# Performance work log

Measured on AMD Instinct MI355X. Metric: run time of the kernel, lower is better.

The kernel has to match this reference:

```python
import jax, jax.numpy as jnp
import numpy as np

VOCAB = 50000
EMB = 128
HID = 128
BEAM = 4
MAXLEN = 24
B = 16
TENC = 64
START_IDX = 2


def setup_inputs() -> dict:
    key = jax.random.key(0)
    ks = jax.random.split(key, 9)
    s = 0.05
    return {
        "encoder_output": jax.random.normal(ks[0], (B, TENC, 2 * HID), jnp.float32),
        "initial_hidden": jax.random.normal(ks[1], (2, B, HID), jnp.float32),
        "embedding": jax.random.normal(ks[2], (VOCAB, EMB), jnp.float32) * s,
        "W_ih": jax.random.normal(ks[3], (3 * HID, EMB), jnp.float32) * s,
        "W_hh": jax.random.normal(ks[4], (3 * HID, HID), jnp.float32) * s,
        "b_ih": jnp.zeros((3 * HID,), jnp.float32),
        "b_hh": jnp.zeros((3 * HID,), jnp.float32),
        "W_logit": jax.random.normal(ks[5], (VOCAB, 2 * HID), jnp.float32) * s,
        "b_logit": jnp.zeros((VOCAB,), jnp.float32),
    }


def _gru_cell(x, h, W_ih, W_hh, b_ih, b_hh):
    # x: [k,B,E], h: [k,B,H]; torch gate order: r, z, n
    gi = x @ W_ih.T + b_ih
    gh = h @ W_hh.T + b_hh
    ir, iz, inn = jnp.split(gi, 3, axis=-1)
    hr, hz, hn = jnp.split(gh, 3, axis=-1)
    r = jax.nn.sigmoid(ir + hr)
    z = jax.nn.sigmoid(iz + hz)
    n = jnp.tanh(inn + r * hn)
    return (1.0 - z) * n + z * h


def _decode(encoder_output, initial_hidden, embedding, W_ih, W_hh, b_ih, b_hh, W_logit, b_logit):
    # take forward-direction encoder states: view(B,T,2,H)[:,:,0,:]
    enc_fwd = encoder_output.reshape(B, TENC, 2, HID)[:, :, 0, :]  # [B,T,H]
    # initial_hidden.view(num_layers=1, 2, B, H)[:,0] -> single-layer fwd hidden
    h0 = initial_hidden.reshape(1, 2, B, HID)[0, 0]  # [B,H]
    k_h0 = jnp.broadcast_to(h0, (BEAM, B, HID))
    k_pred0 = jnp.full((BEAM, B), START_IDX, dtype=jnp.int32)
    k_lps0 = jnp.zeros((BEAM, B), jnp.float32)

    def step(carry, _):
        last_pred, h, lps = carry
        emb = embedding[last_pred]                      # [k,B,E]
        h_new = _gru_cell(emb, h, W_ih, W_hh, b_ih, b_hh)  # [k,B,H]
        out = h_new
        # inline dot attention over forward encoder states
        scores = jnp.einsum('bth,kbh->kbt', enc_fwd, out)      # [k,B,T]
        probs = jax.nn.softmax(scores, axis=-1)
        attn = jnp.einsum('kbt,bth->kbh', probs, enc_fwd)      # [k,B,H]
        feat = jnp.concatenate([attn, out], axis=-1)           # [k,B,2H]
        logits = feat @ W_logit.T + b_logit                    # [k,B,V]
        lsm = jax.nn.log_softmax(logits, axis=-1)
        lps_full = lsm + lps[:, :, None]                       # [k,B,V]
        flat = lps_full.transpose(1, 0, 2).reshape(B, BEAM * VOCAB)
        vals, idx = jax.lax.top_k(flat, BEAM)                  # [B,k]
        beam_idx = idx // VOCAB                                # [B,k]
        tok = (idx % VOCAB).astype(jnp.int32)                  # [B,k]
        # re-sort beam-major tensors by chosen parent beam
        h_b = jnp.take_along_axis(h_new.transpose(1, 0, 2), beam_idx[:, :, None], axis=1).transpose(1, 0, 2)
        lsm_b = jnp.take_along_axis(lsm.transpose(1, 0, 2), beam_idx[:, :, None], axis=1).transpose(1, 0, 2)
        new_carry = (tok.T, h_b, vals.T)
        return new_carry, (lsm_b, tok.T, beam_idx)

    _, (lsm_all, preds_all, parents_all) = jax.lax.scan(
        step, (k_pred0, k_h0, k_lps0), None, length=MAXLEN)
    # lsm_all: [T,k,B,V], preds_all: [T,k,B], parents_all: [T,B,k]

    bidx = jnp.arange(B)

    def back(parent, xs):
        lsm_t, preds_t, parents_t = xs
        out = lsm_t[parent, bidx]          # [B,V]
        pr = preds_t[parent, bidx]         # [B]
        new_parent = parents_t[bidx, parent]
        return new_parent, (out, pr)

    _, (outs, prs) = jax.lax.scan(back, jnp.zeros((B,), jnp.int32),
                                  (lsm_all, preds_all, parents_all), reverse=True)
    return outs, prs  # [T,B,V] log-softmax, [T,B] token ids


def reference(encoder_output, initial_hidden, embedding, W_ih, W_hh, b_ih, b_hh, W_logit, b_logit):
    return _decode(encoder_output, initial_hidden, embedding, W_ih, W_hh, b_ih, b_hh, W_logit, b_logit)
```

## Files before the change

### kernel.cpp

```cpp
#include <hip/hip_runtime.h>
#include <math.h>
#include <float.h>

#define VOCABSZ 50000
#define EMBSZ 128
#define HIDSZ 128
#define BSZ 16
#define TENCSZ 64
#define STEPSN 24
#define STARTTOK 2
#define RPB 64
#define NBLK 782

#define FEAT_OFF 0
#define HBUF_OFF (STEPSN*BSZ*256)
#define CBUF_OFF (HBUF_OFF + BSZ*HIDSZ)
#define PMAX_OFF (CBUF_OFF + STEPSN*BSZ)
#define PSUM_OFF (PMAX_OFF + NBLK*BSZ)
#define WS_FLOATS (PSUM_OFF + NBLK*BSZ)

__global__ __launch_bounds__(256) void step_kernel(
    const float* __restrict__ Wl, const float* __restrict__ bl,
    const float* __restrict__ ws_f_c, float* __restrict__ ws_f,
    int* __restrict__ ws_i, float* __restrict__ out, int t)
{
  const int tid = threadIdx.x;
  const int lane = tid & 63;
  const int waveu = __builtin_amdgcn_readfirstlane(tid >> 6);
  const int r0 = waveu * 4;
  const int v = blockIdx.x * RPB + lane;
  const bool valid = v < VOCABSZ;

  const float* feat_t = ws_f_c + FEAT_OFF + (size_t)t * BSZ * 256;
  const float4* __restrict__ fb = (const float4*)(feat_t + r0 * 256);
  const float4* __restrict__ wrow = (const float4*)(Wl + (size_t)(valid ? v : 0) * 256);

  float a0 = 0.f, a1 = 0.f, a2 = 0.f, a3 = 0.f;
#pragma unroll 4
  for (int k = 0; k < 64; ++k) {
    float4 w = wrow[k];
    float4 f0 = fb[k];
    float4 f1 = fb[64 + k];
    float4 f2 = fb[128 + k];
    float4 f3 = fb[192 + k];
    a0 += f0.x * w.x + f0.y * w.y + f0.z * w.z + f0.w * w.w;
    a1 += f1.x * w.x + f1.y * w.y + f1.z * w.z + f1.w * w.w;
    a2 += f2.x * w.x + f2.y * w.y + f2.z * w.z + f2.w * w.w;
    a3 += f3.x * w.x + f3.y * w.y + f3.z * w.z + f3.w * w.w;
  }
  const float lb = valid ? bl[v] : 0.f;
  float lg[4] = {a0 + lb, a1 + lb, a2 + lb, a3 + lb};

  if (valid) {
#pragma unroll
    for (int j = 0; j < 4; ++j)
      out[((size_t)t * BSZ + (r0 + j)) * VOCABSZ + v] = lg[j];
    if (t > 0) {
      const float* cb = ws_f_c + CBUF_OFF + (t - 1) * BSZ;
#pragma unroll
      for (int j = 0; j < 4; ++j) {
        size_t idx = ((size_t)(t - 1) * BSZ + (r0 + j)) * VOCABSZ + v;
        out[idx] = out[idx] - cb[r0 + j];
      }
    }
  }

  float* pmax = ws_f + PMAX_OFF;
  float* psum = ws_f + PSUM_OFF;
  int* pidx = ws_i;
#pragma unroll
  for (int j = 0; j < 4; ++j) {
    float m = valid ? lg[j] : -FLT_MAX;
    int mi = valid ? v : 0x7fffffff;
#pragma unroll
    for (int off = 32; off; off >>= 1) {
      float om = __shfl_xor(m, off);
      int oi = __shfl_xor(mi, off);
      if (om > m || (om == m && oi < mi)) { m = om; mi = oi; }
    }
    float s = valid ? expf(lg[j] - m) : 0.f;
#pragma unroll
    for (int off = 32; off; off >>= 1) s += __shfl_xor(s, off);
    if (lane == 0) {
      pmax[(r0 + j) * NBLK + blockIdx.x] = m;
      psum[(r0 + j) * NBLK + blockIdx.x] = s;
      pidx[(r0 + j) * NBLK + blockIdx.x] = mi;
    }
  }
}

__global__ __launch_bounds__(256) void rg_kernel(
    const float* __restrict__ enc, const float* __restrict__ inith,
    const float* __restrict__ embed,
    const float* __restrict__ W_ih, const float* __restrict__ W_hh,
    const float* __restrict__ b_ih, const float* __restrict__ b_hh,
    float* __restrict__ ws_f, int* __restrict__ ws_i,
    float* __restrict__ out, int rstep, int gstep)
{
  const int b = blockIdx.x, tid = threadIdx.x;
  float* feat = ws_f + FEAT_OFF;
  float* hbuf = ws_f + HBUF_OFF;
  float* cbuf = ws_f + CBUF_OFF;
  float* pmax = ws_f + PMAX_OFF;
  float* psum = ws_f + PSUM_OFF;
  int* pidx = ws_i;

  __shared__ float s_wm[4]; __shared__ int s_wi[4];
  __shared__ float s_ws[4];
  __shared__ int s_tok;
  __shared__ float s_emb[EMBSZ];
  __shared__ float s_h[HIDSZ];
  __shared__ float s_hnew[HIDSZ];
  __shared__ float s_gh[3 * HIDSZ];
  __shared__ float s_probs[TENCSZ];

  const int lane = tid & 63, wave = tid >> 6;

  if (rstep >= 0) {
    float m = -FLT_MAX; int mi = 0x7fffffff;
    for (int i = tid; i < NBLK; i += 256) {
      float mm = pmax[b * NBLK + i]; int ii = pidx[b * NBLK + i];
      if (mm > m || (mm == m && ii < mi)) { m = mm; mi = ii; }
    }
#pragma unroll
    for (int off = 32; off; off >>= 1) {
      float om = __shfl_xor(m, off); int oi = __shfl_xor(mi, off);
      if (om > m || (om == m && oi < mi)) { m = om; mi = oi; }
    }
    if (lane == 0) { s_wm[wave] = m; s_wi[wave] = mi; }
    __syncthreads();
    float gm = s_wm[0]; int gi_ = s_wi[0];
#pragma unroll
    for (int w = 1; w < 4; ++w) {
      if (s_wm[w] > gm || (s_wm[w] == gm && s_wi[w] < gi_)) { gm = s_wm[w]; gi_ = s_wi[w]; }
    }
    float e = 0.f;
    for (int i = tid; i < NBLK; i += 256)
      e += psum[b * NBLK + i] * expf(pmax[b * NBLK + i] - gm);
#pragma unroll
    for (int off = 32; off; off >>= 1) e += __shfl_xor(e, off);
    if (lane == 0) s_ws[wave] = e;
    __syncthreads();
    if (tid == 0) {
      float tot = s_ws[0] + s_ws[1] + s_ws[2] + s_ws[3];
      cbuf[rstep * BSZ + b] = gm + logf(tot);
      out[(size_t)STEPSN * BSZ * VOCABSZ + rstep * BSZ + b] = (float)gi_;
      s_tok = gi_;
    }
    __syncthreads();
  }

  if (gstep >= 0) {
    const int tok = (gstep == 0) ? STARTTOK : s_tok;
    if (tid < 128) {
      s_emb[tid] = embed[(size_t)tok * EMBSZ + tid];
      s_h[tid] = (gstep == 0) ? inith[b * HIDSZ + tid] : hbuf[b * HIDSZ + tid];
    }
    __syncthreads();
    float gr = 0.f, gz = 0.f, gn = 0.f;
    if (tid < 128) {
      gr = b_ih[tid]; gz = b_ih[tid + 128]; gn = b_ih[tid + 256];
      const float* wr = W_ih + (size_t)tid * EMBSZ;
      const float* wz = W_ih + (size_t)(tid + 128) * EMBSZ;
      const float* wn = W_ih + (size_t)(tid + 256) * EMBSZ;
      for (int k = 0; k < EMBSZ; ++k) {
        float e = s_emb[k];
        gr += wr[k] * e; gz += wz[k] * e; gn += wn[k] * e;
      }
    } else {
      int j = tid - 128;
      float hr = b_hh[j], hz = b_hh[j + 128], hn = b_hh[j + 256];
      const float* wr = W_hh + (size_t)j * HIDSZ;
      const float* wz = W_hh + (size_t)(j + 128) * HIDSZ;
      const float* wn = W_hh + (size_t)(j + 256) * HIDSZ;
      for (int k = 0; k < HIDSZ; ++k) {
        float h = s_h[k];
        hr += wr[k] * h; hz += wz[k] * h; hn += wn[k] * h;
      }
      s_gh[j] = hr; s_gh[128 + j] = hz; s_gh[256 + j] = hn;
    }
    __syncthreads();
    if (tid < 128) {
      float r = 1.f / (1.f + expf(-(gr + s_gh[tid])));
      float z = 1.f / (1.f + expf(-(gz + s_gh[128 + tid])));
      float n = tanhf(gn + r * s_gh[256 + tid]);
      s_hnew[tid] = (1.f - z) * n + z * s_h[tid];
    }
    __syncthreads();
    if (tid < 64) {
      const float* ep = enc + ((size_t)b * TENCSZ + tid) * 256;
      float sc = 0.f;
      for (int k = 0; k < HIDSZ; ++k) sc += ep[k] * s_hnew[k];
      float mx = sc;
#pragma unroll
      for (int off = 32; off; off >>= 1) mx = fmaxf(mx, __shfl_xor(mx, off));
      float p = expf(sc - mx);
      float su = p;
#pragma unroll
      for (int off = 32; off; off >>= 1) su += __shfl_xor(su, off);
      s_probs[tid] = p / su;
    }
    __syncthreads();
    if (tid < 128) {
      float a = 0.f;
      for (int tt = 0; tt < TENCSZ; ++tt)
        a += s_probs[tt] * enc[((size_t)b * TENCSZ + tt) * 256 + tid];
      float* fptr = feat + ((size_t)gstep * BSZ + b) * 256;
      fptr[tid] = a;
      fptr[128 + tid] = s_hnew[tid];
      hbuf[b * HIDSZ + tid] = s_hnew[tid];
    }
  }
}

__global__ __launch_bounds__(256) void sub_last_kernel(
    const float* __restrict__ cbuf, float* __restrict__ out)
{
  size_t i = ((size_t)blockIdx.x * 256 + threadIdx.x) * 8;
  if (i >= (size_t)BSZ * VOCABSZ) return;
  int b = (int)(i / VOCABSZ);
  float c = cbuf[(STEPSN - 1) * BSZ + b];
  float4* p = (float4*)(out + (size_t)(STEPSN - 1) * BSZ * VOCABSZ + i);
  float4 x0 = p[0], x1 = p[1];
  x0.x -= c; x0.y -= c; x0.z -= c; x0.w -= c;
  x1.x -= c; x1.y -= c; x1.z -= c; x1.w -= c;
  p[0] = x0; p[1] = x1;
}

extern "C" void kernel_launch(void* const* d_in, const int* in_sizes, int n_in,
                              void* d_out, int out_size, void* d_ws, size_t ws_size,
                              hipStream_t stream)
{
  const float* enc   = (const float*)d_in[0];
  const float* inith = (const float*)d_in[1];
  const float* embed = (const float*)d_in[2];
  const float* W_ih  = (const float*)d_in[3];
  const float* W_hh  = (const float*)d_in[4];
  const float* b_ih  = (const float*)d_in[5];
  const float* b_hh  = (const float*)d_in[6];
  const float* Wl    = (const float*)d_in[7];
  const float* bl    = (const float*)d_in[8];
  float* out = (float*)d_out;

  float* ws_f = (float*)d_ws;
  int* ws_i = (int*)(ws_f + WS_FLOATS);

  rg_kernel<<<BSZ, 256, 0, stream>>>(enc, inith, embed, W_ih, W_hh, b_ih, b_hh,
                                     ws_f, ws_i, out, -1, 0);
  for (int t = 0; t < STEPSN; ++t) {
    step_kernel<<<NBLK, 256, 0, stream>>>(Wl, bl, ws_f, ws_f, ws_i, out, t);
    rg_kernel<<<BSZ, 256, 0, stream>>>(enc, inith, embed, W_ih, W_hh, b_ih, b_hh,
                                       ws_f, ws_i, out, t, (t < STEPSN - 1) ? (t + 1) : -1);
  }
  const int nsub = (BSZ * VOCABSZ / 8 + 255) / 256;
  sub_last_kernel<<<nsub, 256, 0, stream>>>(ws_f + CBUF_OFF, out);
}
```

Baseline: 1.355 ms.

## Tile logit GEMV through shared memory and stage encoder states in LDS

The vocab logit kernel now gives each block 128 vocab rows. It stages W_logit tiles in double-buffered shared memory with coalesced float4 loads, and each wave computes 8 batch rows instead of 4. This cuts the uncoalesced per-thread row reads of the weight matrix, halves the block count, and doubles the partial softmax slots per block. The recurrent kernel also copies the forward encoder states into LDS once and runs the attention dot products from there with vector reads. The cost is more shared memory per block, which can lower occupancy, plus an extra sync per K tile.

```diff
diff --git a/kernel.cpp b/kernel.cpp
--- a/kernel.cpp
+++ b/kernel.cpp
@@ -9,58 +9,101 @@
 #define TENCSZ 64
 #define STEPSN 24
 #define STARTTOK 2
-#define RPB 64
-#define NBLK 782
+
+#define RPBK 128
+#define NBLK2 391
+#define NSLOT 782
+#define KT 32
+#define PITCH 36
 
 #define FEAT_OFF 0
 #define HBUF_OFF (STEPSN*BSZ*256)
 #define CBUF_OFF (HBUF_OFF + BSZ*HIDSZ)
 #define PMAX_OFF (CBUF_OFF + STEPSN*BSZ)
-#define PSUM_OFF (PMAX_OFF + NBLK*BSZ)
-#define WS_FLOATS (PSUM_OFF + NBLK*BSZ)
+#define PSUM_OFF (PMAX_OFF + NSLOT*BSZ)
+#define WS_FLOATS (PSUM_OFF + NSLOT*BSZ)
 
 __global__ __launch_bounds__(256) void step_kernel(
     const float* __restrict__ Wl, const float* __restrict__ bl,
-    const float* __restrict__ ws_f_c, float* __restrict__ ws_f,
+    const float* __restrict__ ws_c, float* __restrict__ ws_f,
     int* __restrict__ ws_i, float* __restrict__ out, int t)
 {
+  __shared__ float sW[2][RPBK * PITCH];
   const int tid = threadIdx.x;
   const int lane = tid & 63;
-  const int waveu = __builtin_amdgcn_readfirstlane(tid >> 6);
-  const int r0 = waveu * 4;
-  const int v = blockIdx.x * RPB + lane;
+  const int wv = tid >> 6;
+  const int rowhalf = wv & 1;
+  const int bh0 = __builtin_amdgcn_readfirstlane((wv >> 1) * 8);
+  const int v0 = blockIdx.x * RPBK;
+  const int r = rowhalf * 64 + lane;
+  const int v = v0 + r;
   const bool valid = v < VOCABSZ;
 
-  const float* feat_t = ws_f_c + FEAT_OFF + (size_t)t * BSZ * 256;
-  const float4* __restrict__ fb = (const float4*)(feat_t + r0 * 256);
-  const float4* __restrict__ wrow = (const float4*)(Wl + (size_t)(valid ? v : 0) * 256);
-
-  float a0 = 0.f, a1 = 0.f, a2 = 0.f, a3 = 0.f;
-#pragma unroll 4
-  for (int k = 0; k < 64; ++k) {
-    float4 w = wrow[k];
-    float4 f0 = fb[k];
-    float4 f1 = fb[64 + k];
-    float4 f2 = fb[128 + k];
-    float4 f3 = fb[192 + k];
-    a0 += f0.x * w.x + f0.y * w.y + f0.z * w.z + f0.w * w.w;
-    a1 += f1.x * w.x + f1.y * w.y + f1.z * w.z + f1.w * w.w;
-    a2 += f2.x * w.x + f2.y * w.y + f2.z * w.z + f2.w * w.w;
-    a3 += f3.x * w.x + f3.y * w.y + f3.z * w.z + f3.w * w.w;
-  }
+  const float* feat_t = ws_c + FEAT_OFF + (size_t)t * (BSZ * 256) + bh0 * 256;
+  const float4* __restrict__ Wl4 = (const float4*)Wl;
+
+  int srow[4], sc4[4], gbase[4];
+#pragma unroll
+  for (int i = 0; i < 4; ++i) {
+    int f4lin = i * 256 + tid;
+    srow[i] = f4lin >> 3;
+    sc4[i] = f4lin & 7;
+    int vrow = v0 + srow[i];
+    if (vrow >= VOCABSZ) vrow = VOCABSZ - 1;
+    gbase[i] = vrow * 64 + sc4[i];
+  }
+
+  float acc[8];
+#pragma unroll
+  for (int b = 0; b < 8; ++b) acc[b] = 0.f;
+
+  float4 stg[4];
+#pragma unroll
+  for (int i = 0; i < 4; ++i) stg[i] = Wl4[gbase[i]];
+#pragma unroll
+  for (int i = 0; i < 4; ++i)
+    *(float4*)&sW[0][srow[i] * PITCH + sc4[i] * 4] = stg[i];
+  __syncthreads();
+
+  for (int kt = 0; kt < 8; ++kt) {
+    if (kt < 7) {
+#pragma unroll
+      for (int i = 0; i < 4; ++i) stg[i] = Wl4[gbase[i] + (kt + 1) * 8];
+    }
+    const float* wrow = &sW[kt & 1][r * PITCH];
+    const float* fp = feat_t + kt * KT;
+#pragma unroll
+    for (int k4 = 0; k4 < 8; ++k4) {
+      float4 wvv = *(const float4*)&wrow[k4 * 4];
+#pragma unroll
+      for (int b = 0; b < 8; ++b) {
+        float4 f = *(const float4*)(fp + b * 256 + k4 * 4);
+        acc[b] += f.x * wvv.x + f.y * wvv.y + f.z * wvv.z + f.w * wvv.w;
+      }
+    }
+    if (kt < 7) {
+#pragma unroll
+      for (int i = 0; i < 4; ++i)
+        *(float4*)&sW[(kt + 1) & 1][srow[i] * PITCH + sc4[i] * 4] = stg[i];
+      __syncthreads();
+    }
+  }
+
   const float lb = valid ? bl[v] : 0.f;
-  float lg[4] = {a0 + lb, a1 + lb, a2 + lb, a3 + lb};
+  float lg[8];
+#pragma unroll
+  for (int b = 0; b < 8; ++b) lg[b] = acc[b] + lb;
 
   if (valid) {
 #pragma unroll
-    for (int j = 0; j < 4; ++j)
-      out[((size_t)t * BSZ + (r0 + j)) * VOCABSZ + v] = lg[j];
+    for (int b = 0; b < 8; ++b)
+      out[((size_t)t * BSZ + bh0 + b) * VOCABSZ + v] = lg[b];
     if (t > 0) {
-      const float* cb = ws_f_c + CBUF_OFF + (t - 1) * BSZ;
-#pragma unroll
-      for (int j = 0; j < 4; ++j) {
-        size_t idx = ((size_t)(t - 1) * BSZ + (r0 + j)) * VOCABSZ + v;
-        out[idx] = out[idx] - cb[r0 + j];
+      const float* cb = ws_c + CBUF_OFF + (t - 1) * BSZ + bh0;
+#pragma unroll
+      for (int b = 0; b < 8; ++b) {
+        size_t idx = ((size_t)(t - 1) * BSZ + bh0 + b) * VOCABSZ + v;
+        out[idx] = out[idx] - cb[b];
       }
     }
   }
@@ -68,9 +111,10 @@
   float* pmax = ws_f + PMAX_OFF;
   float* psum = ws_f + PSUM_OFF;
   int* pidx = ws_i;
-#pragma unroll
-  for (int j = 0; j < 4; ++j) {
-    float m = valid ? lg[j] : -FLT_MAX;
+  const int slot = blockIdx.x * 2 + rowhalf;
+#pragma unroll
+  for (int b = 0; b < 8; ++b) {
+    float m = valid ? lg[b] : -FLT_MAX;
     int mi = valid ? v : 0x7fffffff;
 #pragma unroll
     for (int off = 32; off; off >>= 1) {
@@ -78,13 +122,13 @@
       int oi = __shfl_xor(mi, off);
       if (om > m || (om == m && oi < mi)) { m = om; mi = oi; }
     }
-    float s = valid ? expf(lg[j] - m) : 0.f;
+    float s = valid ? expf(lg[b] - m) : 0.f;
 #pragma unroll
     for (int off = 32; off; off >>= 1) s += __shfl_xor(s, off);
     if (lane == 0) {
-      pmax[(r0 + j) * NBLK + blockIdx.x] = m;
-      psum[(r0 + j) * NBLK + blockIdx.x] = s;
-      pidx[(r0 + j) * NBLK + blockIdx.x] = mi;
+      pmax[(bh0 + b) * NSLOT + slot] = m;
+      psum[(bh0 + b) * NSLOT + slot] = s;
+      pidx[(bh0 + b) * NSLOT + slot] = mi;
     }
   }
 }
@@ -105,6 +149,7 @@
   float* psum = ws_f + PSUM_OFF;
   int* pidx = ws_i;
 
+  __shared__ float s_enc[64 * 132];
   __shared__ float s_wm[4]; __shared__ int s_wi[4];
   __shared__ float s_ws[4];
   __shared__ int s_tok;
@@ -116,10 +161,20 @@
 
   const int lane = tid & 63, wave = tid >> 6;
 
+  if (gstep >= 0) {
+#pragma unroll
+    for (int i = 0; i < 8; ++i) {
+      int f4lin = i * 256 + tid;
+      int row = f4lin >> 5, c = f4lin & 31;
+      float4 e = ((const float4*)(enc + ((size_t)b * TENCSZ + row) * 256))[c];
+      *(float4*)&s_enc[row * 132 + c * 4] = e;
+    }
+  }
+
   if (rstep >= 0) {
     float m = -FLT_MAX; int mi = 0x7fffffff;
-    for (int i = tid; i < NBLK; i += 256) {
-      float mm = pmax[b * NBLK + i]; int ii = pidx[b * NBLK + i];
+    for (int i = tid; i < NSLOT; i += 256) {
+      float mm = pmax[b * NSLOT + i]; int ii = pidx[b * NSLOT + i];
       if (mm > m || (mm == m && ii < mi)) { m = mm; mi = ii; }
     }
 #pragma unroll
@@ -135,8 +190,8 @@
       if (s_wm[w] > gm || (s_wm[w] == gm && s_wi[w] < gi_)) { gm = s_wm[w]; gi_ = s_wi[w]; }
     }
     float e = 0.f;
-    for (int i = tid; i < NBLK; i += 256)
-      e += psum[b * NBLK + i] * expf(pmax[b * NBLK + i] - gm);
+    for (int i = tid; i < NSLOT; i += 256)
+      e += psum[b * NSLOT + i] * expf(pmax[b * NSLOT + i] - gm);
 #pragma unroll
     for (int off = 32; off; off >>= 1) e += __shfl_xor(e, off);
     if (lane == 0) s_ws[wave] = e;
@@ -188,9 +243,14 @@
     }
     __syncthreads();
     if (tid < 64) {
-      const float* ep = enc + ((size_t)b * TENCSZ + tid) * 256;
+      const float4* ep = (const float4*)&s_enc[tid * 132];
+      const float4* h4 = (const float4*)s_hnew;
       float sc = 0.f;
-      for (int k = 0; k < HIDSZ; ++k) sc += ep[k] * s_hnew[k];
+#pragma unroll
+      for (int k = 0; k < 32; ++k) {
+        float4 e = ep[k], h = h4[k];
+        sc += e.x * h.x + e.y * h.y + e.z * h.z + e.w * h.w;
+      }
       float mx = sc;
 #pragma unroll
       for (int off = 32; off; off >>= 1) mx = fmaxf(mx, __shfl_xor(mx, off));
@@ -203,8 +263,9 @@
     __syncthreads();
     if (tid < 128) {
       float a = 0.f;
+#pragma unroll 8
       for (int tt = 0; tt < TENCSZ; ++tt)
-        a += s_probs[tt] * enc[((size_t)b * TENCSZ + tt) * 256 + tid];
+        a += s_probs[tt] * s_enc[tt * 132 + tid];
       float* fptr = feat + ((size_t)gstep * BSZ + b) * 256;
       fptr[tid] = a;
       fptr[128 + tid] = s_hnew[tid];
@@ -248,7 +309,7 @@
   rg_kernel<<<BSZ, 256, 0, stream>>>(enc, inith, embed, W_ih, W_hh, b_ih, b_hh,
                                      ws_f, ws_i, out, -1, 0);
   for (int t = 0; t < STEPSN; ++t) {
-    step_kernel<<<NBLK, 256, 0, stream>>>(Wl, bl, ws_f, ws_f, ws_i, out, t);
+    step_kernel<<<NBLK2, 256, 0, stream>>>(Wl, bl, ws_f, ws_f, ws_i, out, t);
     rg_kernel<<<BSZ, 256, 0, stream>>>(enc, inith, embed, W_ih, W_hh, b_ih, b_hh,
                                        ws_f, ws_i, out, t, (t < STEPSN - 1) ? (t + 1) : -1);
   }
```

Result: slower. 1.701 ms (+25.5%).

## Fuse per-step reduction and GRU into logit kernel via last-block atomic ticket

Applied to the files above, without the earlier changes.

Merges the separate reduce/GRU kernel into the logit step kernel: each block takes an atomic ticket, and the last 16 blocks spin until all blocks finish, then each performs the argmax/logsumexp reduction and next-step GRU+attention for one batch row. The logit GEMV is restructured so each wave computes 16 vocab rows for all 16 batch rows, with 8 lanes splitting K, so each weight row is read once per step instead of four times. This removes one launch per step and the redundant weight traffic, at the cost of spin-waiting blocks, larger partial buffers, and more registers.

```diff
diff --git a/kernel.cpp b/kernel.cpp
--- a/kernel.cpp
+++ b/kernel.cpp
@@ -9,208 +9,268 @@
 #define TENCSZ 64
 #define STEPSN 24
 #define STARTTOK 2
-#define RPB 64
+
+#define ROWSB 64
 #define NBLK 782
+#define NSLOT (NBLK*4)
 
 #define FEAT_OFF 0
 #define HBUF_OFF (STEPSN*BSZ*256)
 #define CBUF_OFF (HBUF_OFF + BSZ*HIDSZ)
 #define PMAX_OFF (CBUF_OFF + STEPSN*BSZ)
-#define PSUM_OFF (PMAX_OFF + NBLK*BSZ)
-#define WS_FLOATS (PSUM_OFF + NBLK*BSZ)
+#define PSUM_OFF (PMAX_OFF + NSLOT*BSZ)
+#define WS_FLOATS (PSUM_OFF + NSLOT*BSZ)
+
+__device__ __forceinline__ void gru_attn(
+    int tid, int b, int tok, int gstep,
+    const float* __restrict__ enc, const float* __restrict__ inith,
+    const float* __restrict__ embed,
+    const float* __restrict__ W_ih, const float* __restrict__ W_hh,
+    const float* __restrict__ b_ih, const float* __restrict__ b_hh,
+    float* __restrict__ ws_f,
+    float* s_emb, float* s_h, float* s_hnew, float* s_hg, float* s_probs)
+{
+  if (tid < 128) {
+    s_emb[tid] = embed[(size_t)tok * EMBSZ + tid];
+    s_h[tid] = (gstep == 0) ? inith[b * HIDSZ + tid]
+                            : (ws_f + HBUF_OFF)[b * HIDSZ + tid];
+  }
+  __syncthreads();
+  float xr = 0.f, xz = 0.f, xn = 0.f;
+  if (tid < 128) {
+    xr = b_ih[tid]; xz = b_ih[tid + 128]; xn = b_ih[tid + 256];
+    const float4* wr = (const float4*)(W_ih + (size_t)tid * EMBSZ);
+    const float4* wz = (const float4*)(W_ih + (size_t)(tid + 128) * EMBSZ);
+    const float4* wn = (const float4*)(W_ih + (size_t)(tid + 256) * EMBSZ);
+    const float4* e4 = (const float4*)s_emb;
+#pragma unroll 8
+    for (int k = 0; k < 32; ++k) {
+      float4 e = e4[k], a = wr[k], bq = wz[k], cq = wn[k];
+      xr += a.x * e.x + a.y * e.y + a.z * e.z + a.w * e.w;
+      xz += bq.x * e.x + bq.y * e.y + bq.z * e.z + bq.w * e.w;
+      xn += cq.x * e.x + cq.y * e.y + cq.z * e.z + cq.w * e.w;
+    }
+  } else {
+    int j = tid - 128;
+    float hr = b_hh[j], hz = b_hh[j + 128], hn = b_hh[j + 256];
+    const float4* wr = (const float4*)(W_hh + (size_t)j * HIDSZ);
+    const float4* wz = (const float4*)(W_hh + (size_t)(j + 128) * HIDSZ);
+    const float4* wn = (const float4*)(W_hh + (size_t)(j + 256) * HIDSZ);
+    const float4* h4 = (const float4*)s_h;
+    float a1 = 0.f, a2 = 0.f, a3 = 0.f;
+#pragma unroll 8
+    for (int k = 0; k < 32; ++k) {
+      float4 h = h4[k], a = wr[k], bq = wz[k], cq = wn[k];
+      a1 += a.x * h.x + a.y * h.y + a.z * h.z + a.w * h.w;
+      a2 += bq.x * h.x + bq.y * h.y + bq.z * h.z + bq.w * h.w;
+      a3 += cq.x * h.x + cq.y * h.y + cq.z * h.z + cq.w * h.w;
+    }
+    s_hg[j] = hr + a1; s_hg[128 + j] = hz + a2; s_hg[256 + j] = hn + a3;
+  }
+  __syncthreads();
+  if (tid < 128) {
+    float r = 1.f / (1.f + expf(-(xr + s_hg[tid])));
+    float z = 1.f / (1.f + expf(-(xz + s_hg[128 + tid])));
+    float n = tanhf(xn + r * s_hg[256 + tid]);
+    s_hnew[tid] = (1.f - z) * n + z * s_h[tid];
+  }
+  __syncthreads();
+  if (tid < 64) {
+    const float4* ep = (const float4*)(enc + ((size_t)b * TENCSZ + tid) * 256);
+    const float4* h4 = (const float4*)s_hnew;
+    float sc = 0.f;
+#pragma unroll 8
+    for (int k = 0; k < 32; ++k) {
+      float4 e = ep[k], h = h4[k];
+      sc += e.x * h.x + e.y * h.y + e.z * h.z + e.w * h.w;
+    }
+    float mx = sc;
+#pragma unroll
+    for (int off = 32; off; off >>= 1) mx = fmaxf(mx, __shfl_xor(mx, off));
+    float p = expf(sc - mx);
+    float su = p;
+#pragma unroll
+    for (int off = 32; off; off >>= 1) su += __shfl_xor(su, off);
+    s_probs[tid] = p / su;
+  }
+  __syncthreads();
+  if (tid < 128) {
+    float a = 0.f;
+#pragma unroll 8
+    for (int tt = 0; tt < TENCSZ; ++tt)
+      a += s_probs[tt] * enc[((size_t)b * TENCSZ + tt) * 256 + tid];
+    float* fptr = ws_f + FEAT_OFF + ((size_t)gstep * BSZ + b) * 256;
+    fptr[tid] = a;
+    fptr[128 + tid] = s_hnew[tid];
+    (ws_f + HBUF_OFF)[b * HIDSZ + tid] = s_hnew[tid];
+  }
+}
 
 __global__ __launch_bounds__(256) void step_kernel(
     const float* __restrict__ Wl, const float* __restrict__ bl,
-    const float* __restrict__ ws_f_c, float* __restrict__ ws_f,
-    int* __restrict__ ws_i, float* __restrict__ out, int t)
-{
-  const int tid = threadIdx.x;
-  const int lane = tid & 63;
-  const int waveu = __builtin_amdgcn_readfirstlane(tid >> 6);
-  const int r0 = waveu * 4;
-  const int v = blockIdx.x * RPB + lane;
-  const bool valid = v < VOCABSZ;
-
-  const float* feat_t = ws_f_c + FEAT_OFF + (size_t)t * BSZ * 256;
-  const float4* __restrict__ fb = (const float4*)(feat_t + r0 * 256);
-  const float4* __restrict__ wrow = (const float4*)(Wl + (size_t)(valid ? v : 0) * 256);
-
-  float a0 = 0.f, a1 = 0.f, a2 = 0.f, a3 = 0.f;
-#pragma unroll 4
-  for (int k = 0; k < 64; ++k) {
-    float4 w = wrow[k];
-    float4 f0 = fb[k];
-    float4 f1 = fb[64 + k];
-    float4 f2 = fb[128 + k];
-    float4 f3 = fb[192 + k];
-    a0 += f0.x * w.x + f0.y * w.y + f0.z * w.z + f0.w * w.w;
-    a1 += f1.x * w.x + f1.y * w.y + f1.z * w.z + f1.w * w.w;
-    a2 += f2.x * w.x + f2.y * w.y + f2.z * w.z + f2.w * w.w;
-    a3 += f3.x * w.x + f3.y * w.y + f3.z * w.z + f3.w * w.w;
-  }
-  const float lb = valid ? bl[v] : 0.f;
-  float lg[4] = {a0 + lb, a1 + lb, a2 + lb, a3 + lb};
-
-  if (valid) {
-#pragma unroll
-    for (int j = 0; j < 4; ++j)
-      out[((size_t)t * BSZ + (r0 + j)) * VOCABSZ + v] = lg[j];
-    if (t > 0) {
-      const float* cb = ws_f_c + CBUF_OFF + (t - 1) * BSZ;
-#pragma unroll
-      for (int j = 0; j < 4; ++j) {
-        size_t idx = ((size_t)(t - 1) * BSZ + (r0 + j)) * VOCABSZ + v;
-        out[idx] = out[idx] - cb[r0 + j];
-      }
-    }
-  }
-
-  float* pmax = ws_f + PMAX_OFF;
-  float* psum = ws_f + PSUM_OFF;
-  int* pidx = ws_i;
-#pragma unroll
-  for (int j = 0; j < 4; ++j) {
-    float m = valid ? lg[j] : -FLT_MAX;
-    int mi = valid ? v : 0x7fffffff;
-#pragma unroll
-    for (int off = 32; off; off >>= 1) {
-      float om = __shfl_xor(m, off);
-      int oi = __shfl_xor(mi, off);
-      if (om > m || (om == m && oi < mi)) { m = om; mi = oi; }
-    }
-    float s = valid ? expf(lg[j] - m) : 0.f;
-#pragma unroll
-    for (int off = 32; off; off >>= 1) s += __shfl_xor(s, off);
-    if (lane == 0) {
-      pmax[(r0 + j) * NBLK + blockIdx.x] = m;
-      psum[(r0 + j) * NBLK + blockIdx.x] = s;
-      pidx[(r0 + j) * NBLK + blockIdx.x] = mi;
-    }
-  }
-}
-
-__global__ __launch_bounds__(256) void rg_kernel(
     const float* __restrict__ enc, const float* __restrict__ inith,
     const float* __restrict__ embed,
     const float* __restrict__ W_ih, const float* __restrict__ W_hh,
     const float* __restrict__ b_ih, const float* __restrict__ b_hh,
     float* __restrict__ ws_f, int* __restrict__ ws_i,
-    float* __restrict__ out, int rstep, int gstep)
-{
-  const int b = blockIdx.x, tid = threadIdx.x;
-  float* feat = ws_f + FEAT_OFF;
-  float* hbuf = ws_f + HBUF_OFF;
-  float* cbuf = ws_f + CBUF_OFF;
+    float* __restrict__ out, int t)
+{
+  __shared__ float s_emb[EMBSZ], s_h[HIDSZ], s_hnew[HIDSZ];
+  __shared__ float s_hg[3 * HIDSZ], s_probs[TENCSZ];
+  __shared__ float s_rm[4], s_rs[4]; __shared__ int s_ri[4];
+  __shared__ int s_ticket; __shared__ float s_gm; __shared__ int s_gi, s_tok;
+
+  int* pidx = ws_i;
+  int* ctr = ws_i + NSLOT * BSZ;
   float* pmax = ws_f + PMAX_OFF;
   float* psum = ws_f + PSUM_OFF;
-  int* pidx = ws_i;
-
-  __shared__ float s_wm[4]; __shared__ int s_wi[4];
-  __shared__ float s_ws[4];
-  __shared__ int s_tok;
-  __shared__ float s_emb[EMBSZ];
-  __shared__ float s_h[HIDSZ];
-  __shared__ float s_hnew[HIDSZ];
-  __shared__ float s_gh[3 * HIDSZ];
-  __shared__ float s_probs[TENCSZ];
-
-  const int lane = tid & 63, wave = tid >> 6;
-
-  if (rstep >= 0) {
-    float m = -FLT_MAX; int mi = 0x7fffffff;
-    for (int i = tid; i < NBLK; i += 256) {
-      float mm = pmax[b * NBLK + i]; int ii = pidx[b * NBLK + i];
-      if (mm > m || (mm == m && ii < mi)) { m = mm; mi = ii; }
-    }
-#pragma unroll
-    for (int off = 32; off; off >>= 1) {
+
+  const int tid = threadIdx.x;
+  const int lane = tid & 63;
+  const int w = tid >> 6;
+  const int r0 = lane >> 3;
+  const int c = lane & 7;
+  const int v1 = blockIdx.x * ROWSB + w * 16 + r0;
+  const int v2 = v1 + 8;
+  const bool val1 = v1 < VOCABSZ, val2 = v2 < VOCABSZ;
+  const int v1c = val1 ? v1 : 0;
+  const int v2c = val2 ? v2 : 0;
+
+  const float4* F4 = (const float4*)(ws_f + FEAT_OFF + (size_t)t * (BSZ * 256));
+  const float4* W4 = (const float4*)Wl;
+  const int a1 = v1c * 64 + c;
+  const int a2 = v2c * 64 + c;
+
+  float acc1[BSZ], acc2[BSZ];
+#pragma unroll
+  for (int b = 0; b < BSZ; ++b) { acc1[b] = 0.f; acc2[b] = 0.f; }
+
+#pragma unroll
+  for (int i = 0; i < 8; ++i) {
+    float4 w1 = W4[a1 + i * 8];
+    float4 w2 = W4[a2 + i * 8];
+#pragma unroll
+    for (int b = 0; b < BSZ; ++b) {
+      float4 f = F4[b * 64 + i * 8 + c];
+      acc1[b] += f.x * w1.x + f.y * w1.y + f.z * w1.z + f.w * w1.w;
+      acc2[b] += f.x * w2.x + f.y * w2.y + f.z * w2.z + f.w * w2.w;
+    }
+  }
+#pragma unroll
+  for (int off = 1; off <= 4; off <<= 1) {
+#pragma unroll
+    for (int b = 0; b < BSZ; ++b) {
+      acc1[b] += __shfl_xor(acc1[b], off);
+      acc2[b] += __shfl_xor(acc2[b], off);
+    }
+  }
+  const float lb1 = bl[v1c], lb2 = bl[v2c];
+  const float* cb = ws_f + CBUF_OFF + (t - 1) * BSZ;
+  const int slot = blockIdx.x * 4 + w;
+
+#pragma unroll
+  for (int b = 0; b < BSZ; ++b) {
+    float lg1 = acc1[b] + lb1;
+    float lg2 = acc2[b] + lb2;
+    if ((b & 7) == c) {
+      if (val1) out[((size_t)t * BSZ + b) * VOCABSZ + v1] = lg1;
+      if (val2) out[((size_t)t * BSZ + b) * VOCABSZ + v2] = lg2;
+      if (t > 0) {
+        float cv = cb[b];
+        if (val1) { size_t i1 = ((size_t)(t - 1) * BSZ + b) * VOCABSZ + v1; out[i1] -= cv; }
+        if (val2) { size_t i2 = ((size_t)(t - 1) * BSZ + b) * VOCABSZ + v2; out[i2] -= cv; }
+      }
+    }
+    float m; int mi;
+    if (val1) { m = lg1; mi = v1; } else { m = -FLT_MAX; mi = 0x7fffffff; }
+    if (val2 && lg2 > m) { m = lg2; mi = v2; }
+#pragma unroll
+    for (int off = 8; off <= 32; off <<= 1) {
       float om = __shfl_xor(m, off); int oi = __shfl_xor(mi, off);
       if (om > m || (om == m && oi < mi)) { m = om; mi = oi; }
     }
-    if (lane == 0) { s_wm[wave] = m; s_wi[wave] = mi; }
-    __syncthreads();
-    float gm = s_wm[0]; int gi_ = s_wi[0];
-#pragma unroll
-    for (int w = 1; w < 4; ++w) {
-      if (s_wm[w] > gm || (s_wm[w] == gm && s_wi[w] < gi_)) { gm = s_wm[w]; gi_ = s_wi[w]; }
-    }
-    float e = 0.f;
-    for (int i = tid; i < NBLK; i += 256)
-      e += psum[b * NBLK + i] * expf(pmax[b * NBLK + i] - gm);
-#pragma unroll
-    for (int off = 32; off; off >>= 1) e += __shfl_xor(e, off);
-    if (lane == 0) s_ws[wave] = e;
-    __syncthreads();
-    if (tid == 0) {
-      float tot = s_ws[0] + s_ws[1] + s_ws[2] + s_ws[3];
-      cbuf[rstep * BSZ + b] = gm + logf(tot);
-      out[(size_t)STEPSN * BSZ * VOCABSZ + rstep * BSZ + b] = (float)gi_;
-      s_tok = gi_;
-    }
-    __syncthreads();
-  }
-
-  if (gstep >= 0) {
-    const int tok = (gstep == 0) ? STARTTOK : s_tok;
-    if (tid < 128) {
-      s_emb[tid] = embed[(size_t)tok * EMBSZ + tid];
-      s_h[tid] = (gstep == 0) ? inith[b * HIDSZ + tid] : hbuf[b * HIDSZ + tid];
-    }
-    __syncthreads();
-    float gr = 0.f, gz = 0.f, gn = 0.f;
-    if (tid < 128) {
-      gr = b_ih[tid]; gz = b_ih[tid + 128]; gn = b_ih[tid + 256];
-      const float* wr = W_ih + (size_t)tid * EMBSZ;
-      const float* wz = W_ih + (size_t)(tid + 128) * EMBSZ;
-      const float* wn = W_ih + (size_t)(tid + 256) * EMBSZ;
-      for (int k = 0; k < EMBSZ; ++k) {
-        float e = s_emb[k];
-        gr += wr[k] * e; gz += wz[k] * e; gn += wn[k] * e;
-      }
-    } else {
-      int j = tid - 128;
-      float hr = b_hh[j], hz = b_hh[j + 128], hn = b_hh[j + 256];
-      const float* wr = W_hh + (size_t)j * HIDSZ;
-      const float* wz = W_hh + (size_t)(j + 128) * HIDSZ;
-      const float* wn = W_hh + (size_t)(j + 256) * HIDSZ;
-      for (int k = 0; k < HIDSZ; ++k) {
-        float h = s_h[k];
-        hr += wr[k] * h; hz += wz[k] * h; hn += wn[k] * h;
-      }
-      s_gh[j] = hr; s_gh[128 + j] = hz; s_gh[256 + j] = hn;
-    }
-    __syncthreads();
-    if (tid < 128) {
-      float r = 1.f / (1.f + expf(-(gr + s_gh[tid])));
-      float z = 1.f / (1.f + expf(-(gz + s_gh[128 + tid])));
-      float n = tanhf(gn + r * s_gh[256 + tid]);
-      s_hnew[tid] = (1.f - z) * n + z * s_h[tid];
-    }
-    __syncthreads();
-    if (tid < 64) {
-      const float* ep = enc + ((size_t)b * TENCSZ + tid) * 256;
-      float sc = 0.f;
-      for (int k = 0; k < HIDSZ; ++k) sc += ep[k] * s_hnew[k];
-      float mx = sc;
-#pragma unroll
-      for (int off = 32; off; off >>= 1) mx = fmaxf(mx, __shfl_xor(mx, off));
-      float p = expf(sc - mx);
-      float su = p;
-#pragma unroll
-      for (int off = 32; off; off >>= 1) su += __shfl_xor(su, off);
-      s_probs[tid] = p / su;
-    }
-    __syncthreads();
-    if (tid < 128) {
-      float a = 0.f;
-      for (int tt = 0; tt < TENCSZ; ++tt)
-        a += s_probs[tt] * enc[((size_t)b * TENCSZ + tt) * 256 + tid];
-      float* fptr = feat + ((size_t)gstep * BSZ + b) * 256;
-      fptr[tid] = a;
-      fptr[128 + tid] = s_hnew[tid];
-      hbuf[b * HIDSZ + tid] = s_hnew[tid];
-    }
-  }
+    float s = (val1 ? __expf(lg1 - m) : 0.f) + (val2 ? __expf(lg2 - m) : 0.f);
+#pragma unroll
+    for (int off = 8; off <= 32; off <<= 1) s += __shfl_xor(s, off);
+    if (lane == b) {
+      pmax[b * NSLOT + slot] = m;
+      psum[b * NSLOT + slot] = s;
+      pidx[b * NSLOT + slot] = mi;
+    }
+  }
+
+  __syncthreads();
+  if (tid == 0)
+    s_ticket = __hip_atomic_fetch_add(ctr + t, 1, __ATOMIC_RELEASE,
+                                      __HIP_MEMORY_SCOPE_AGENT);
+  __syncthreads();
+  const int ticket = s_ticket;
+  if (ticket < NBLK - BSZ) return;
+  const int b = ticket - (NBLK - BSZ);
+
+  if (tid == 0) {
+    while (__hip_atomic_load(ctr + t, __ATOMIC_ACQUIRE,
+                             __HIP_MEMORY_SCOPE_AGENT) < NBLK)
+      __builtin_amdgcn_s_sleep(2);
+  }
+  __syncthreads();
+
+  float m = -FLT_MAX; int mi = 0x7fffffff;
+  for (int i = tid; i < NSLOT; i += 256) {
+    float mm = pmax[b * NSLOT + i]; int ii = pidx[b * NSLOT + i];
+    if (mm > m || (mm == m && ii < mi)) { m = mm; mi = ii; }
+  }
+#pragma unroll
+  for (int off = 32; off; off >>= 1) {
+    float om = __shfl_xor(m, off); int oi = __shfl_xor(mi, off);
+    if (om > m || (om == m && oi < mi)) { m = om; mi = oi; }
+  }
+  if (lane == 0) { s_rm[w] = m; s_ri[w] = mi; }
+  __syncthreads();
+  if (tid == 0) {
+    float gm = s_rm[0]; int gi = s_ri[0];
+#pragma unroll
+    for (int q = 1; q < 4; ++q)
+      if (s_rm[q] > gm || (s_rm[q] == gm && s_ri[q] < gi)) { gm = s_rm[q]; gi = s_ri[q]; }
+    s_gm = gm; s_gi = gi;
+  }
+  __syncthreads();
+  const float gm = s_gm;
+
+  float s = 0.f;
+  for (int i = tid; i < NSLOT; i += 256)
+    s += psum[b * NSLOT + i] * __expf(pmax[b * NSLOT + i] - gm);
+#pragma unroll
+  for (int off = 32; off; off >>= 1) s += __shfl_xor(s, off);
+  if (lane == 0) s_rs[w] = s;
+  __syncthreads();
+  if (tid == 0) {
+    float tot = s_rs[0] + s_rs[1] + s_rs[2] + s_rs[3];
+    (ws_f + CBUF_OFF)[t * BSZ + b] = gm + logf(tot);
+    out[(size_t)STEPSN * BSZ * VOCABSZ + t * BSZ + b] = (float)s_gi;
+    s_tok = s_gi;
+  }
+  __syncthreads();
+
+  if (t < STEPSN - 1) {
+    gru_attn(tid, b, s_tok, t + 1, enc, inith, embed, W_ih, W_hh, b_ih, b_hh,
+             ws_f, s_emb, s_h, s_hnew, s_hg, s_probs);
+  }
+}
+
+__global__ __launch_bounds__(256) void feat0_kernel(
+    const float* __restrict__ enc, const float* __restrict__ inith,
+    const float* __restrict__ embed,
+    const float* __restrict__ W_ih, const float* __restrict__ W_hh,
+    const float* __restrict__ b_ih, const float* __restrict__ b_hh,
+    float* __restrict__ ws_f, int* __restrict__ ws_i)
+{
+  __shared__ float s_emb[EMBSZ], s_h[HIDSZ], s_hnew[HIDSZ];
+  __shared__ float s_hg[3 * HIDSZ], s_probs[TENCSZ];
+  if (blockIdx.x == 0 && threadIdx.x < 32)
+    (ws_i + NSLOT * BSZ)[threadIdx.x] = 0;
+  gru_attn(threadIdx.x, blockIdx.x, STARTTOK, 0, enc, inith, embed,
+           W_ih, W_hh, b_ih, b_hh, ws_f, s_emb, s_h, s_hnew, s_hg, s_probs);
 }
 
 __global__ __launch_bounds__(256) void sub_last_kernel(
@@ -219,11 +279,11 @@
   size_t i = ((size_t)blockIdx.x * 256 + threadIdx.x) * 8;
   if (i >= (size_t)BSZ * VOCABSZ) return;
   int b = (int)(i / VOCABSZ);
-  float c = cbuf[(STEPSN - 1) * BSZ + b];
+  float cv = cbuf[(STEPSN - 1) * BSZ + b];
   float4* p = (float4*)(out + (size_t)(STEPSN - 1) * BSZ * VOCABSZ + i);
   float4 x0 = p[0], x1 = p[1];
-  x0.x -= c; x0.y -= c; x0.z -= c; x0.w -= c;
-  x1.x -= c; x1.y -= c; x1.z -= c; x1.w -= c;
+  x0.x -= cv; x0.y -= cv; x0.z -= cv; x0.w -= cv;
+  x1.x -= cv; x1.y -= cv; x1.z -= cv; x1.w -= cv;
   p[0] = x0; p[1] = x1;
 }
 
@@ -245,12 +305,12 @@
   float* ws_f = (float*)d_ws;
   int* ws_i = (int*)(ws_f + WS_FLOATS);
 
-  rg_kernel<<<BSZ, 256, 0, stream>>>(enc, inith, embed, W_ih, W_hh, b_ih, b_hh,
-                                     ws_f, ws_i, out, -1, 0);
+  feat0_kernel<<<BSZ, 256, 0, stream>>>(enc, inith, embed, W_ih, W_hh,
+                                        b_ih, b_hh, ws_f, ws_i);
   for (int t = 0; t < STEPSN; ++t) {
-    step_kernel<<<NBLK, 256, 0, stream>>>(Wl, bl, ws_f, ws_f, ws_i, out, t);
-    rg_kernel<<<BSZ, 256, 0, stream>>>(enc, inith, embed, W_ih, W_hh, b_ih, b_hh,
-                                       ws_f, ws_i, out, t, (t < STEPSN - 1) ? (t + 1) : -1);
+    step_kernel<<<NBLK, 256, 0, stream>>>(Wl, bl, enc, inith, embed,
+                                          W_ih, W_hh, b_ih, b_hh,
+                                          ws_f, ws_i, out, t);
   }
   const int nsub = (BSZ * VOCABSZ / 8 + 255) / 256;
   sub_last_kernel<<<nsub, 256, 0, stream>>>(ws_f + CBUF_OFF, out);
```

After: 2.771 ms. 2.05x slower.
